# Kernel optimization log

Hardware: AMD Instinct MI355X
Metric: run time of the kernel (lower is better)

Reference implementation:

```python
import jax, jax.numpy as jnp
import numpy as np

N_NODES = 50000
N_EDGES = 800000
IN_F, E_F, OUT_F = 128, 32, 128

def setup_inputs() -> dict:
    key = jax.random.key(0)
    ks = jax.random.split(key, 8)
    return {
        "h": jax.random.normal(ks[0], (N_NODES, IN_F), dtype=jnp.float32),
        "eftr": jax.random.normal(ks[1], (N_EDGES, E_F), dtype=jnp.float32),
        "weight": jax.random.normal(ks[2], (IN_F + E_F, OUT_F), dtype=jnp.float32) * (1.0 / np.sqrt(IN_F + E_F)),
        "W_w": jax.random.normal(ks[3], (OUT_F, IN_F + OUT_F), dtype=jnp.float32) * (1.0 / np.sqrt(IN_F + OUT_F)),
        "W_b": jax.random.normal(ks[4], (OUT_F,), dtype=jnp.float32) * 0.01,
        "bias": jnp.zeros((OUT_F,), dtype=jnp.float32),
        "src_idx": jax.random.randint(ks[5], (N_EDGES,), 0, N_NODES, dtype=jnp.int64) if jax.config.jax_enable_x64 else jax.random.randint(ks[5], (N_EDGES,), 0, N_NODES, dtype=jnp.int32),
        "dst_idx": jax.random.randint(ks[6], (N_EDGES,), 0, N_NODES, dtype=jnp.int32),
        "num_dst": N_NODES,
    }

def reference(h, eftr, weight, W_w, W_b, bias, src_idx, dst_idx, num_dst):
    # Segment-mean of concat([h[src], eftr]) over dst neighborhoods.
    # Sum node part and edge part separately (avoids materializing the concat mailbox).
    sum_h = jax.ops.segment_sum(h[src_idx], dst_idx, num_segments=num_dst)   # [D, IN_F]
    sum_e = jax.ops.segment_sum(eftr, dst_idx, num_segments=num_dst)        # [D, E_F]
    cnt = jax.ops.segment_sum(jnp.ones((dst_idx.shape[0],), h.dtype), dst_idx, num_segments=num_dst)
    denom = jnp.maximum(cnt, 1.0)[:, None]  # zero-degree nodes -> h_neigh = 0
    feat_mean = jnp.concatenate([sum_h / denom, sum_e / denom], axis=-1)    # [D, IN_F+E_F]
    h_neigh = feat_mean @ weight                                            # [D, OUT_F]
    h_dst = h[:num_dst]
    h_prime = jnp.concatenate([h_dst, h_neigh], axis=1) @ W_w.T + W_b       # Linear W
    h_prime = h_prime + bias
    return h_prime
```

## Files before the change

### kernel.cpp

```cpp
#include <hip/hip_runtime.h>

#define NN   50000
#define NE   800000
#define INF  128
#define EF   32
#define OUTF 128
#define KDIM 288
#define NBLK ((NN + 1023) / 1024)

typedef __attribute__((ext_vector_type(8))) short     short8;
typedef __attribute__((ext_vector_type(8))) unsigned short ushort8;
typedef __attribute__((ext_vector_type(4))) float     float4v;

__device__ __forceinline__ unsigned short f2bf(float f) {
    union { float f; unsigned int u; } c; c.f = f;
    const unsigned int r = (c.u + 0x7FFFu + ((c.u >> 16) & 1u)) >> 16;
    return (unsigned short)r;
}

__global__ void prep_kernel(const float* __restrict__ weight,
                            const float* __restrict__ W_w,
                            const float* __restrict__ W_b,
                            const float* __restrict__ bias,
                            float* __restrict__ Mmat,
                            float* __restrict__ cvec) {
    __shared__ float wrow[OUTF];
    const int r = blockIdx.x;
    const int j = threadIdx.x;
    if (r < 128) {
        Mmat[r * OUTF + j] = W_w[j * 256 + r];
        return;
    }
    if (r == KDIM) {
        cvec[j] = W_b[j] + bias[j];
        return;
    }
    const int m = r - 128;
    wrow[j] = weight[m * OUTF + j];
    __syncthreads();
    float acc = 0.f;
#pragma unroll 8
    for (int k = 0; k < OUTF; ++k)
        acc += wrow[k] * W_w[j * 256 + 128 + k];
    Mmat[r * OUTF + j] = acc;
}

__global__ void pack_kernel(const float* __restrict__ Mmat,
                            unsigned short* __restrict__ Mb) {
    const int b = blockIdx.x;
    const int kb = b >> 3;
    const int ct = b & 7;
    const int lane = threadIdx.x;
    const int col = ct * 16 + (lane & 15);
    const int k0 = kb * 32 + (lane >> 4) * 8;
    ushort8 v;
#pragma unroll
    for (int i = 0; i < 8; ++i)
        v[i] = f2bf(Mmat[(size_t)(k0 + i) * OUTF + col]);
    *(ushort8*)(Mb + ((size_t)(b * 64 + lane) * 8)) = v;
}

__global__ __launch_bounds__(256)
void hist_kernel(const int* __restrict__ dst, int* __restrict__ off) {
    const int e = blockIdx.x * 256 + threadIdx.x;
    if (e < NE) atomicAdd(&off[dst[e]], 1);
}

__global__ __launch_bounds__(256)
void scan1_kernel(const int* __restrict__ off, int* __restrict__ partial) {
    const int b = blockIdx.x;
    const int tid = threadIdx.x;
    const int idx = b * 1024 + tid * 4;
    int v0 = 0, v1 = 0, v2 = 0, v3 = 0;
    if (idx + 3 < NN) {
        const int4 q = *(const int4*)(off + idx);
        v0 = q.x; v1 = q.y; v2 = q.z; v3 = q.w;
    } else {
        if (idx + 0 < NN) v0 = off[idx + 0];
        if (idx + 1 < NN) v1 = off[idx + 1];
        if (idx + 2 < NN) v2 = off[idx + 2];
    }
    int t = v0 + v1 + v2 + v3;
#pragma unroll
    for (int ofs = 32; ofs > 0; ofs >>= 1) t += __shfl_down(t, ofs);
    __shared__ int wsum[4];
    if ((tid & 63) == 0) wsum[tid >> 6] = t;
    __syncthreads();
    if (tid == 0) partial[b] = wsum[0] + wsum[1] + wsum[2] + wsum[3];
}

__global__ __launch_bounds__(256)
void scan3_kernel(int* __restrict__ off, const int* __restrict__ partial) {
    __shared__ int blockbase;
    __shared__ int wsum[4];
    const int b = blockIdx.x;
    const int tid = threadIdx.x;
    const int lane = tid & 63;
    const int wid = tid >> 6;

    if (wid == 0) {
        const int v = (lane < NBLK) ? partial[lane] : 0;
        int x = v;
#pragma unroll
        for (int ofs = 1; ofs < 64; ofs <<= 1) {
            const int t = __shfl_up(x, ofs);
            if (lane >= ofs) x += t;
        }
        if (lane == b) blockbase = x - v;
    }

    const int idx = b * 1024 + tid * 4;
    int v0 = 0, v1 = 0, v2 = 0, v3 = 0;
    if (idx + 3 < NN) {
        const int4 q = *(const int4*)(off + idx);
        v0 = q.x; v1 = q.y; v2 = q.z; v3 = q.w;
    } else {
        if (idx + 0 < NN) v0 = off[idx + 0];
        if (idx + 1 < NN) v1 = off[idx + 1];
        if (idx + 2 < NN) v2 = off[idx + 2];
    }
    const int tsum = v0 + v1 + v2 + v3;
    int x = tsum;
#pragma unroll
    for (int ofs = 1; ofs < 64; ofs <<= 1) {
        const int t = __shfl_up(x, ofs);
        if (lane >= ofs) x += t;
    }
    if (lane == 63) wsum[wid] = x;
    __syncthreads();
    int wp = 0;
    for (int w = 0; w < wid; ++w) wp += wsum[w];
    const int base = blockbase + wp + (x - tsum);
    if (idx + 0 < NN) off[idx + 0] = base;
    if (idx + 1 < NN) off[idx + 1] = base + v0;
    if (idx + 2 < NN) off[idx + 2] = base + v0 + v1;
    if (idx + 3 < NN) off[idx + 3] = base + v0 + v1 + v2;
}

__global__ __launch_bounds__(256)
void scatter_ids_kernel(const int* __restrict__ srcv,
                        const int* __restrict__ dst,
                        int* __restrict__ off,
                        int2* __restrict__ eo2) {
    const int e = blockIdx.x * 256 + threadIdx.x;
    if (e < NE) {
        const int d = dst[e];
        const int pos = atomicAdd(&off[d], 1);
        eo2[pos] = make_int2(srcv[e], e);
    }
}

__global__ __launch_bounds__(256)
void gather_kernel(const float* __restrict__ h,
                   const float* __restrict__ eftr,
                   const int* __restrict__ off,
                   const int2* __restrict__ eo2,
                   float* __restrict__ mean_h,
                   float* __restrict__ mean_e) {
    const int tid = threadIdx.x;
    const int lane = tid & 63;
    const int node = blockIdx.x * 4 + (tid >> 6);
    if (node >= NN) return;

    const int end = off[node];
    const int start = (node == 0) ? 0 : off[node - 1];

    float ax = 0.f, ay = 0.f, ae = 0.f;
    const float* hcol = h + lane * 2;
    const int el = lane & 31;
    const bool lowhalf = (lane < 32);

    for (int base = start; base < end; base += 64) {
        const int m = min(64, end - base);
        int px = 0, py = 0;
        if (base + lane < end) {
            const long long pv =
                __builtin_nontemporal_load((const long long*)(eo2 + base + lane));
            px = (int)pv;
            py = (int)(pv >> 32);
        }
        int j = 0;
        for (; j + 7 < m; j += 8) {
            int s[8], e[8];
#pragma unroll
            for (int u = 0; u < 8; ++u) {
                s[u] = __builtin_amdgcn_readlane(px, j + u);
                e[u] = __builtin_amdgcn_readlane(py, j + u);
            }
            float2 v[8];
#pragma unroll
            for (int u = 0; u < 8; ++u)
                v[u] = *(const float2*)(hcol + (size_t)s[u] * INF);
            float f[4];
#pragma unroll
            for (int u = 0; u < 4; ++u) {
                const int ee = lowhalf ? e[2 * u] : e[2 * u + 1];
                f[u] = __builtin_nontemporal_load(&eftr[(size_t)ee * EF + el]);
            }
#pragma unroll
            for (int u = 0; u < 8; ++u) { ax += v[u].x; ay += v[u].y; }
            ae += (f[0] + f[1]) + (f[2] + f[3]);
        }
        for (; j < m; ++j) {
            const int s0 = __builtin_amdgcn_readlane(px, j);
            const int e0 = __builtin_amdgcn_readlane(py, j);
            const float2 v0 = *(const float2*)(hcol + (size_t)s0 * INF);
            ax += v0.x;
            ay += v0.y;
            if (lowhalf) ae += __builtin_nontemporal_load(&eftr[(size_t)e0 * EF + el]);
        }
    }

    ae += __shfl(ae, lane + 32);

    const float inv = 1.f / fmaxf((float)(end - start), 1.f);
    *(float2*)(mean_h + (size_t)node * INF + lane * 2) =
        make_float2(ax * inv, ay * inv);
    if (lowhalf) mean_e[(size_t)node * EF + el] = ae * inv;
}

__global__ __launch_bounds__(256)
void node_gemm_kernel(const float* __restrict__ h,
                      const float* __restrict__ mean_h,
                      const float* __restrict__ mean_e,
                      const unsigned short* __restrict__ Mb,
                      const float* __restrict__ cvec,
                      float* __restrict__ out) {
    const int tid = threadIdx.x;
    const int lane = tid & 63;
    const int wid = tid >> 6;
    const int nt = blockIdx.x * 4 + wid;
    const int m16 = lane & 15;
    const int quad = lane >> 4;
    const int koff = quad * 8;

    const int anode = nt * 16 + m16;
    const int nclamp = (anode < NN) ? anode : (NN - 1);

    float4v acc[8] = {};

    for (int kb = 0; kb < 9; ++kb) {
        const float* srcp;
        if (kb < 4)
            srcp = h + (size_t)nclamp * INF + kb * 32 + koff;
        else if (kb < 8)
            srcp = mean_h + (size_t)nclamp * INF + (kb - 4) * 32 + koff;
        else
            srcp = mean_e + (size_t)nclamp * EF + koff;
        const float4 p0 = *(const float4*)srcp;
        const float4 p1 = *(const float4*)(srcp + 4);
        short8 a;
        a[0] = (short)f2bf(p0.x); a[1] = (short)f2bf(p0.y);
        a[2] = (short)f2bf(p0.z); a[3] = (short)f2bf(p0.w);
        a[4] = (short)f2bf(p1.x); a[5] = (short)f2bf(p1.y);
        a[6] = (short)f2bf(p1.z); a[7] = (short)f2bf(p1.w);

        const short8* bp = (const short8*)(Mb + (size_t)kb * 8 * 64 * 8);
#pragma unroll
        for (int ct = 0; ct < 8; ++ct) {
            const short8 b = bp[ct * 64 + lane];
            acc[ct] = __builtin_amdgcn_mfma_f32_16x16x32_bf16(a, b, acc[ct], 0, 0, 0);
        }
    }

    float cv[8];
#pragma unroll
    for (int ct = 0; ct < 8; ++ct) cv[ct] = cvec[ct * 16 + m16];

#pragma unroll
    for (int r = 0; r < 4; ++r) {
        const int nrow = nt * 16 + quad * 4 + r;
        if (nrow < NN) {
            float* orow = out + (size_t)nrow * OUTF;
#pragma unroll
            for (int ct = 0; ct < 8; ++ct)
                orow[ct * 16 + m16] = acc[ct][r] + cv[ct];
        }
    }
}

extern "C" void kernel_launch(void* const* d_in, const int* in_sizes, int n_in,
                              void* d_out, int out_size, void* d_ws, size_t ws_size,
                              hipStream_t stream) {
    const float* h      = (const float*)d_in[0];
    const float* eftr   = (const float*)d_in[1];
    const float* weight = (const float*)d_in[2];
    const float* W_w    = (const float*)d_in[3];
    const float* W_b    = (const float*)d_in[4];
    const float* bias   = (const float*)d_in[5];
    const int*   src    = (const int*)d_in[6];
    const int*   dst    = (const int*)d_in[7];
    float* out = (float*)d_out;

    float* ws      = (float*)d_ws;
    float* mean_h  = ws;
    float* mean_e  = mean_h + (size_t)NN * INF;
    float* Mmat    = mean_e + (size_t)NN * EF;
    float* cvec    = Mmat + (size_t)KDIM * OUTF;
    unsigned short* Mb = (unsigned short*)(cvec + OUTF);
    int*   off     = (int*)((char*)Mb + (size_t)9 * 8 * 64 * 8 * 2);
    int2*  eo2     = (int2*)(off + NN);
    int*   partial = (int*)(eo2 + NE);

    hipMemsetAsync(off, 0, (size_t)NN * sizeof(int), stream);

    prep_kernel<<<KDIM + 1, 128, 0, stream>>>(weight, W_w, W_b, bias, Mmat, cvec);
    pack_kernel<<<72, 64, 0, stream>>>(Mmat, Mb);
    hist_kernel<<<(NE + 255) / 256, 256, 0, stream>>>(dst, off);
    scan1_kernel<<<NBLK, 256, 0, stream>>>(off, partial);
    scan3_kernel<<<NBLK, 256, 0, stream>>>(off, partial);
    scatter_ids_kernel<<<(NE + 255) / 256, 256, 0, stream>>>(src, dst, off, eo2);
    gather_kernel<<<(NN + 3) / 4, 256, 0, stream>>>(h, eftr, off, eo2,
                                                    mean_h, mean_e);
    node_gemm_kernel<<<(NN / 64) + 1, 256, 0, stream>>>(h, mean_h, mean_e,
                                                        Mb, cvec, out);
}
```

Before: 341.4 us.

## Store neighbor means as bf16, widen gather loads, fuse weight prep and pack

The gather kernel now reads h rows as float4 with two edges per wavefront half, reads edge features as float4 with eight edges per iteration, and reduces across lanes with shuffles. It writes the means directly as bf16, so the GEMM kernel loads them without converting and the intermediate traffic is halved. The weight-fold and bf16-pack kernels are merged into one launch that recomputes dot products per element. The histogram kernel now handles four destinations per thread. The risks are precision loss from storing the means in bf16 before the GEMM and redundant dot products in the prep kernel.

```diff
diff --git a/kernel.cpp b/kernel.cpp
--- a/kernel.cpp
+++ b/kernel.cpp
@@ -8,9 +8,10 @@
 #define KDIM 288
 #define NBLK ((NN + 1023) / 1024)
 
-typedef __attribute__((ext_vector_type(8))) short     short8;
+typedef __attribute__((ext_vector_type(8))) short          short8;
 typedef __attribute__((ext_vector_type(8))) unsigned short ushort8;
-typedef __attribute__((ext_vector_type(4))) float     float4v;
+typedef __attribute__((ext_vector_type(4))) unsigned short ushort4v;
+typedef __attribute__((ext_vector_type(4))) float          float4v;
 
 __device__ __forceinline__ unsigned short f2bf(float f) {
     union { float f; unsigned int u; } c; c.f = f;
@@ -18,52 +19,58 @@
     return (unsigned short)r;
 }
 
-__global__ void prep_kernel(const float* __restrict__ weight,
-                            const float* __restrict__ W_w,
-                            const float* __restrict__ W_b,
-                            const float* __restrict__ bias,
-                            float* __restrict__ Mmat,
-                            float* __restrict__ cvec) {
-    __shared__ float wrow[OUTF];
-    const int r = blockIdx.x;
-    const int j = threadIdx.x;
-    if (r < 128) {
-        Mmat[r * OUTF + j] = W_w[j * 256 + r];
+__global__ void prep_pack_kernel(const float* __restrict__ weight,
+                                 const float* __restrict__ W_w,
+                                 const float* __restrict__ W_b,
+                                 const float* __restrict__ bias,
+                                 unsigned short* __restrict__ Mb,
+                                 float* __restrict__ cvec) {
+    const int b = blockIdx.x;
+    const int lane = threadIdx.x;
+    if (b == 72) {
+        cvec[lane]      = W_b[lane]      + bias[lane];
+        cvec[lane + 64] = W_b[lane + 64] + bias[lane + 64];
         return;
     }
-    if (r == KDIM) {
-        cvec[j] = W_b[j] + bias[j];
-        return;
-    }
-    const int m = r - 128;
-    wrow[j] = weight[m * OUTF + j];
-    __syncthreads();
-    float acc = 0.f;
-#pragma unroll 8
-    for (int k = 0; k < OUTF; ++k)
-        acc += wrow[k] * W_w[j * 256 + 128 + k];
-    Mmat[r * OUTF + j] = acc;
-}
-
-__global__ void pack_kernel(const float* __restrict__ Mmat,
-                            unsigned short* __restrict__ Mb) {
-    const int b = blockIdx.x;
     const int kb = b >> 3;
     const int ct = b & 7;
-    const int lane = threadIdx.x;
     const int col = ct * 16 + (lane & 15);
     const int k0 = kb * 32 + (lane >> 4) * 8;
     ushort8 v;
 #pragma unroll
-    for (int i = 0; i < 8; ++i)
-        v[i] = f2bf(Mmat[(size_t)(k0 + i) * OUTF + col]);
+    for (int i = 0; i < 8; ++i) {
+        const int k = k0 + i;
+        float val;
+        if (k < 128) {
+            val = W_w[(size_t)col * 256 + k];
+        } else {
+            const float4* wr  = (const float4*)(weight + (size_t)(k - 128) * OUTF);
+            const float4* wwr = (const float4*)(W_w + (size_t)col * 256 + 128);
+            float acc = 0.f;
+#pragma unroll 4
+            for (int c = 0; c < 32; ++c) {
+                const float4 a = wr[c], bb = wwr[c];
+                acc += a.x * bb.x + a.y * bb.y + a.z * bb.z + a.w * bb.w;
+            }
+            val = acc;
+        }
+        v[i] = f2bf(val);
+    }
     *(ushort8*)(Mb + ((size_t)(b * 64 + lane) * 8)) = v;
 }
 
 __global__ __launch_bounds__(256)
 void hist_kernel(const int* __restrict__ dst, int* __restrict__ off) {
-    const int e = blockIdx.x * 256 + threadIdx.x;
-    if (e < NE) atomicAdd(&off[dst[e]], 1);
+    const int e = (blockIdx.x * 256 + threadIdx.x) * 4;
+    if (e + 3 < NE) {
+        const int4 d = *(const int4*)(dst + e);
+        atomicAdd(&off[d.x], 1);
+        atomicAdd(&off[d.y], 1);
+        atomicAdd(&off[d.z], 1);
+        atomicAdd(&off[d.w], 1);
+    } else {
+        for (int i = e; i < NE; ++i) atomicAdd(&off[dst[i]], 1);
+    }
 }
 
 __global__ __launch_bounds__(256)
@@ -155,8 +162,8 @@
                    const float* __restrict__ eftr,
                    const int* __restrict__ off,
                    const int2* __restrict__ eo2,
-                   float* __restrict__ mean_h,
-                   float* __restrict__ mean_e) {
+                   unsigned short* __restrict__ mean_h,
+                   unsigned short* __restrict__ mean_e) {
     const int tid = threadIdx.x;
     const int lane = tid & 63;
     const int node = blockIdx.x * 4 + (tid >> 6);
@@ -165,10 +172,13 @@
     const int end = off[node];
     const int start = (node == 0) ? 0 : off[node - 1];
 
-    float ax = 0.f, ay = 0.f, ae = 0.f;
-    const float* hcol = h + lane * 2;
-    const int el = lane & 31;
-    const bool lowhalf = (lane < 32);
+    const int half = lane >> 5;
+    const int hcol = (lane & 31) * 4;
+    const int g = lane >> 3;
+    const int ecol = (lane & 7) * 4;
+
+    float4 ah = make_float4(0.f, 0.f, 0.f, 0.f);
+    float4 ae = make_float4(0.f, 0.f, 0.f, 0.f);
 
     for (int base = start; base < end; base += 64) {
         const int m = min(64, end - base);
@@ -179,50 +189,58 @@
             px = (int)pv;
             py = (int)(pv >> 32);
         }
-        int j = 0;
-        for (; j + 7 < m; j += 8) {
-            int s[8], e[8];
-#pragma unroll
-            for (int u = 0; u < 8; ++u) {
-                s[u] = __builtin_amdgcn_readlane(px, j + u);
-                e[u] = __builtin_amdgcn_readlane(py, j + u);
+        for (int j = 0; j < m; j += 8) {
+            float4 hv[4];
+            bool hok[4];
+#pragma unroll
+            for (int u = 0; u < 4; ++u) {
+                const int ei = j + 2 * u + half;
+                const int s = __shfl(px, ei);
+                hv[u] = *(const float4*)(h + (size_t)s * INF + hcol);
+                hok[u] = (ei < m);
             }
-            float2 v[8];
-#pragma unroll
-            for (int u = 0; u < 8; ++u)
-                v[u] = *(const float2*)(hcol + (size_t)s[u] * INF);
-            float f[4];
-#pragma unroll
-            for (int u = 0; u < 4; ++u) {
-                const int ee = lowhalf ? e[2 * u] : e[2 * u + 1];
-                f[u] = __builtin_nontemporal_load(&eftr[(size_t)ee * EF + el]);
+            const int ee = __shfl(py, j + g);
+            const float4 fv = *(const float4*)(eftr + (size_t)ee * EF + ecol);
+            const bool eok = (j + g < m);
+#pragma unroll
+            for (int u = 0; u < 4; ++u)
+                if (hok[u]) {
+                    ah.x += hv[u].x; ah.y += hv[u].y;
+                    ah.z += hv[u].z; ah.w += hv[u].w;
+                }
+            if (eok) {
+                ae.x += fv.x; ae.y += fv.y; ae.z += fv.z; ae.w += fv.w;
             }
-#pragma unroll
-            for (int u = 0; u < 8; ++u) { ax += v[u].x; ay += v[u].y; }
-            ae += (f[0] + f[1]) + (f[2] + f[3]);
-        }
-        for (; j < m; ++j) {
-            const int s0 = __builtin_amdgcn_readlane(px, j);
-            const int e0 = __builtin_amdgcn_readlane(py, j);
-            const float2 v0 = *(const float2*)(hcol + (size_t)s0 * INF);
-            ax += v0.x;
-            ay += v0.y;
-            if (lowhalf) ae += __builtin_nontemporal_load(&eftr[(size_t)e0 * EF + el]);
-        }
-    }
-
-    ae += __shfl(ae, lane + 32);
+        }
+    }
+
+    ah.x += __shfl_xor(ah.x, 32); ah.y += __shfl_xor(ah.y, 32);
+    ah.z += __shfl_xor(ah.z, 32); ah.w += __shfl_xor(ah.w, 32);
+#pragma unroll
+    for (int d = 8; d <= 32; d <<= 1) {
+        ae.x += __shfl_xor(ae.x, d); ae.y += __shfl_xor(ae.y, d);
+        ae.z += __shfl_xor(ae.z, d); ae.w += __shfl_xor(ae.w, d);
+    }
 
     const float inv = 1.f / fmaxf((float)(end - start), 1.f);
-    *(float2*)(mean_h + (size_t)node * INF + lane * 2) =
-        make_float2(ax * inv, ay * inv);
-    if (lowhalf) mean_e[(size_t)node * EF + el] = ae * inv;
+    if (lane < 32) {
+        ushort4v o;
+        o[0] = f2bf(ah.x * inv); o[1] = f2bf(ah.y * inv);
+        o[2] = f2bf(ah.z * inv); o[3] = f2bf(ah.w * inv);
+        *(ushort4v*)(mean_h + (size_t)node * INF + hcol) = o;
+    }
+    if (lane < 8) {
+        ushort4v o;
+        o[0] = f2bf(ae.x * inv); o[1] = f2bf(ae.y * inv);
+        o[2] = f2bf(ae.z * inv); o[3] = f2bf(ae.w * inv);
+        *(ushort4v*)(mean_e + (size_t)node * EF + ecol) = o;
+    }
 }
 
 __global__ __launch_bounds__(256)
 void node_gemm_kernel(const float* __restrict__ h,
-                      const float* __restrict__ mean_h,
-                      const float* __restrict__ mean_e,
+                      const unsigned short* __restrict__ mean_h,
+                      const unsigned short* __restrict__ mean_e,
                       const unsigned short* __restrict__ Mb,
                       const float* __restrict__ cvec,
                       float* __restrict__ out) {
@@ -240,20 +258,20 @@
     float4v acc[8] = {};
 
     for (int kb = 0; kb < 9; ++kb) {
-        const float* srcp;
-        if (kb < 4)
-            srcp = h + (size_t)nclamp * INF + kb * 32 + koff;
-        else if (kb < 8)
-            srcp = mean_h + (size_t)nclamp * INF + (kb - 4) * 32 + koff;
-        else
-            srcp = mean_e + (size_t)nclamp * EF + koff;
-        const float4 p0 = *(const float4*)srcp;
-        const float4 p1 = *(const float4*)(srcp + 4);
         short8 a;
-        a[0] = (short)f2bf(p0.x); a[1] = (short)f2bf(p0.y);
-        a[2] = (short)f2bf(p0.z); a[3] = (short)f2bf(p0.w);
-        a[4] = (short)f2bf(p1.x); a[5] = (short)f2bf(p1.y);
-        a[6] = (short)f2bf(p1.z); a[7] = (short)f2bf(p1.w);
+        if (kb < 4) {
+            const float* srcp = h + (size_t)nclamp * INF + kb * 32 + koff;
+            const float4 p0 = *(const float4*)srcp;
+            const float4 p1 = *(const float4*)(srcp + 4);
+            a[0] = (short)f2bf(p0.x); a[1] = (short)f2bf(p0.y);
+            a[2] = (short)f2bf(p0.z); a[3] = (short)f2bf(p0.w);
+            a[4] = (short)f2bf(p1.x); a[5] = (short)f2bf(p1.y);
+            a[6] = (short)f2bf(p1.z); a[7] = (short)f2bf(p1.w);
+        } else if (kb < 8) {
+            a = *(const short8*)(mean_h + (size_t)nclamp * INF + (kb - 4) * 32 + koff);
+        } else {
+            a = *(const short8*)(mean_e + (size_t)nclamp * EF + koff);
+        }
 
         const short8* bp = (const short8*)(Mb + (size_t)kb * 8 * 64 * 8);
 #pragma unroll
@@ -292,21 +310,19 @@
     const int*   dst    = (const int*)d_in[7];
     float* out = (float*)d_out;
 
-    float* ws      = (float*)d_ws;
-    float* mean_h  = ws;
-    float* mean_e  = mean_h + (size_t)NN * INF;
-    float* Mmat    = mean_e + (size_t)NN * EF;
-    float* cvec    = Mmat + (size_t)KDIM * OUTF;
-    unsigned short* Mb = (unsigned short*)(cvec + OUTF);
-    int*   off     = (int*)((char*)Mb + (size_t)9 * 8 * 64 * 8 * 2);
-    int2*  eo2     = (int2*)(off + NN);
-    int*   partial = (int*)(eo2 + NE);
+    char* p = (char*)d_ws;
+    unsigned short* mean_h = (unsigned short*)p;  p += (size_t)NN * INF * 2;
+    unsigned short* mean_e = (unsigned short*)p;  p += (size_t)NN * EF * 2;
+    unsigned short* Mb     = (unsigned short*)p;  p += (size_t)KDIM * OUTF * 2;
+    float*          cvec   = (float*)p;          p += OUTF * 4;
+    int*            off    = (int*)p;            p += (size_t)NN * 4;
+    int2*           eo2    = (int2*)p;           p += (size_t)NE * 8;
+    int*            partial= (int*)p;
 
     hipMemsetAsync(off, 0, (size_t)NN * sizeof(int), stream);
 
-    prep_kernel<<<KDIM + 1, 128, 0, stream>>>(weight, W_w, W_b, bias, Mmat, cvec);
-    pack_kernel<<<72, 64, 0, stream>>>(Mmat, Mb);
-    hist_kernel<<<(NE + 255) / 256, 256, 0, stream>>>(dst, off);
+    prep_pack_kernel<<<73, 64, 0, stream>>>(weight, W_w, W_b, bias, Mb, cvec);
+    hist_kernel<<<(NE / 4 + 255) / 256, 256, 0, stream>>>(dst, off);
     scan1_kernel<<<NBLK, 256, 0, stream>>>(off, partial);
     scan3_kernel<<<NBLK, 256, 0, stream>>>(off, partial);
     scatter_ids_kernel<<<(NE + 255) / 256, 256, 0, stream>>>(src, dst, off, eo2);
```

New measurement: 352.2 us. 1.03x slower.
